# Performance work log

Measured on AMD Instinct MI355X. Metric: run time of the kernel, lower is better.

Reference implementation:

```python
import jax, jax.numpy as jnp
import numpy as np

G, N = 1024, 40            # graphs, nodes per graph (complete graphs)
SLOPE = 0.1                # leaky relu negative slope
SMAT_IDX = jnp.array([0, 1, 2, 3, 1, 4, 5, 6, 2, 5, 7, 8, 3, 6, 8, 9])


def setup_inputs() -> dict:
    key = jax.random.key(0)
    ks = jax.random.split(key, 24)

    # --- graph structure: G identical complete graphs of N nodes ---
    ii, jj = np.meshgrid(np.arange(N), np.arange(N), indexing="ij")
    mask = ii != jj
    src_l, dst_l = ii[mask], jj[mask]              # directed edges per graph
    offs = (np.arange(G) * N)[:, None]
    edge_index = np.stack([(src_l[None] + offs).ravel(),
                           (dst_l[None] + offs).ravel()]).astype(np.int64)
    iu, ju = np.triu_indices(N, 1)
    M = iu.shape[0]                                 # 780 undirected edges
    ud_edges = np.stack([iu, ju], 1).astype(np.int64)
    edge_map = np.zeros((N, N), np.int64)
    edge_map[iu, ju] = np.arange(M)
    edge_map[ju, iu] = np.arange(M)

    def w(k, shape, fan_in):
        return jax.random.normal(k, shape, jnp.float32) / np.sqrt(fan_in)

    inp = {
        "x": jax.random.normal(ks[0], (G * N, 16), jnp.float32),
        "edge_index": jnp.asarray(edge_index),
        "ud_edges": jnp.asarray(ud_edges),
        "edge_map": jnp.asarray(edge_map),
        # GCN stack 6->32->32->64
        "Wg0": w(ks[1], (6, 32), 6),   "bg0": jnp.zeros((32,), jnp.float32),
        "Wg1": w(ks[2], (32, 32), 32), "bg1": jnp.zeros((32,), jnp.float32),
        "Wg2": w(ks[3], (32, 64), 32), "bg2": jnp.zeros((64,), jnp.float32),
        # node MLP 64->64->64->10
        "Wn0": w(ks[4], (64, 64), 64), "bn0": jnp.zeros((64,), jnp.float32),
        "Wn1": w(ks[5], (64, 64), 64), "bn1": jnp.zeros((64,), jnp.float32),
        "Wn2": w(ks[6], (64, 10), 64), "bn2": jnp.zeros((10,), jnp.float32),
        # edge MLP 64->64->64->10
        "We0": w(ks[7], (64, 64), 64), "be0": jnp.zeros((64,), jnp.float32),
        "We1": w(ks[8], (64, 64), 64), "be1": jnp.zeros((64,), jnp.float32),
        "We2": w(ks[9], (64, 10), 64), "be2": jnp.zeros((10,), jnp.float32),
    }
    return inp


def _forward(x, edge_index, ud_edges, edge_map,
             Wg0, bg0, Wg1, bg1, Wg2, bg2,
             Wn0, bn0, Wn1, bn1, Wn2, bn2,
             We0, be0, We1, be1, We2, be2):
    num_nodes = x.shape[0]
    h = x[:, :6]                                   # node_feature_mode == 1
    src, dst = edge_index[0], edge_index[1]

    # GCN normalization (add_self_loops=False, edge_weight=1)
    deg = jax.ops.segment_sum(jnp.ones(src.shape[0], x.dtype), dst,
                              num_segments=num_nodes)
    dis = jnp.where(deg > 0, jax.lax.rsqrt(jnp.maximum(deg, 1e-12)), 0.0)
    norm = dis[src] * dis[dst]                     # [E]

    def gcn(h, W, b):
        m = (h @ W)[src] * norm[:, None]
        return jax.ops.segment_sum(m, dst, num_segments=num_nodes) + b

    # eval mode: dropout is identity
    h = jax.nn.leaky_relu(gcn(h, Wg0, bg0), SLOPE)
    h = jax.nn.leaky_relu(gcn(h, Wg1, bg1), SLOPE)
    h = gcn(h, Wg2, bg2)                           # [G*N, 64]

    hg = h.reshape(G, N, -1)                       # [G, N, 64]

    def mlp(z, Ws, bs):
        for W, b in zip(Ws[:-1], bs[:-1]):
            z = jax.nn.leaky_relu(z @ W + b, SLOPE)
        return z @ Ws[-1] + bs[-1]

    vp = mlp(hg, [Wn0, Wn1, Wn2], [bn0, bn1, bn2])            # [G, N, 10]
    e = hg[:, ud_edges[:, 0], :] + hg[:, ud_edges[:, 1], :]   # [G, M, 64]
    ep = mlp(e, [We0, We1, We2], [be0, be1, be2])             # [G, M, 10]

    # recover_X: diag blocks smat(vp[i]), off-diag smat(ep[edge_map[i,j]])
    epm = ep[:, edge_map, :]                                  # [G, N, N, 10]
    eye = jnp.eye(N, dtype=bool)[None, :, :, None]
    vecs = jnp.where(eye, vp[:, :, None, :], epm)             # [G, N, N, 10]
    blocks = vecs[..., SMAT_IDX].reshape(G, N, N, 4, 4)
    X = blocks.transpose(0, 1, 3, 2, 4).reshape(G, 4 * N, 4 * N)
    return h, X


def reference(x, edge_index, ud_edges, edge_map,
              Wg0, bg0, Wg1, bg1, Wg2, bg2,
              Wn0, bn0, Wn1, bn1, Wn2, bn2,
              We0, be0, We1, be1, We2, be2):
    return _forward(x, edge_index, ud_edges, edge_map,
                    Wg0, bg0, Wg1, bg1, Wg2, bg2,
                    Wn0, bn0, Wn1, bn1, Wn2, bn2,
                    We0, be0, We1, be1, We2, be2)
```

## Files before the change

### kernel.cpp

```cpp
#include <hip/hip_runtime.h>

#define G_GRAPHS 1024
#define N_NODES  40
#define M_EDGES  780
#define NUM_NODES (G_GRAPHS * N_NODES)
#define H_ELEMS  (NUM_NODES * 64)
#define X_STRIDE 160
#define X_PER_G  25600
#define SLOPE 0.1f

#define PACK_PER_MLP 9216

typedef __bf16 bf16x8 __attribute__((ext_vector_type(8)));
typedef unsigned short us8 __attribute__((ext_vector_type(8)));
typedef float f32x4 __attribute__((ext_vector_type(4)));

__device__ __forceinline__ float lrelu(float v) { return fmaxf(v, SLOPE * v); }
__device__ __forceinline__ unsigned short f2bf(float x) {
    __bf16 b = (__bf16)x;
    return __builtin_bit_cast(unsigned short, b);
}
__device__ __forceinline__ unsigned int pk2bf(float a, float b) {
    return (unsigned int)f2bf(a) | ((unsigned int)f2bf(b) << 16);
}

__global__ __launch_bounds__(256) void k_prep(const float* __restrict__ We0,
                                              const float* __restrict__ We1,
                                              const float* __restrict__ We2,
                                              const float* __restrict__ Wn0,
                                              const float* __restrict__ Wn1,
                                              const float* __restrict__ Wn2,
                                              unsigned short* __restrict__ wp) {
    int t = blockIdx.x * 256 + threadIdx.x;
    int mlp = t / PACK_PER_MLP;
    int o = t - mlp * PACK_PER_MLP;
    const float* W0 = mlp ? Wn0 : We0;
    const float* W1 = mlp ? Wn1 : We1;
    const float* W2 = mlp ? Wn2 : We2;
    float val;
    if (o < 8192) {
        const float* W = (o < 4096) ? W0 : W1;
        int idx = o & 4095;
        int j = idx & 7, l = (idx >> 3) & 63, tt = idx >> 9;
        int kt = tt & 1, mt = tt >> 1;
        int k = kt * 32 + ((l >> 4) & 3) * 8 + j;
        int m = mt * 16 + (l & 15);
        val = W[k * 64 + m];
    } else {
        int idx = o - 8192;
        int j = idx & 7, l = (idx >> 3) & 63, kt = idx >> 9;
        int k = kt * 32 + ((l >> 4) & 3) * 8 + j;
        int m = l & 15;
        val = (m < 10) ? W2[k * 10 + m] : 0.f;
    }
    wp[mlp * PACK_PER_MLP + o] = f2bf(val);
}

struct ChunkRegs {
    bf16x8 A1[4][2];
    bf16x8 A2[4][2];
    bf16x8 A3[2];
    float4 bv0[4];
    float4 bv1[4];
    float  bz[4];
};

__device__ __forceinline__ void run_pair(int R0A, int R0B, int w, int l,
                                         const float4* sh4,
                                         unsigned short* sBA,
                                         unsigned short* sBB,
                                         float* sEP,
                                         const unsigned short* sIJ,
                                         const ChunkRegs& cr) {
    const int nl = l & 15;
    const int rq = (l >> 4) & 3;
    const int rl = l >> 1;
    const int hf2 = l & 1;

    auto decode = [&](int row, int& ii, int& jj, bool& is_e, bool& is_n) {
        is_e = (row < 780);
        is_n = (row >= 800 && row < 840);
        ii = 0; jj = 0;
        if (is_e) {
            unsigned short e = sIJ[row];
            ii = e >> 8; jj = e & 255;
        } else if (is_n) {
            ii = jj = row - 800;
        }
    };
    int iiA, jjA, iiB, jjB; bool ieA, inA, ieB, inB;
    decode(R0A + rl, iiA, jjA, ieA, inA);
    decode(R0B + rl, iiB, jjB, ieB, inB);

    auto ebuild = [&](unsigned short* sB, int ii, int jj, bool is_e) {
        unsigned short tmp[32];
#pragma unroll
        for (int q = 0; q < 8; q++) {
            int u = hf2 * 8 + q;
            float4 a = sh4[ii * 16 + (u ^ ((ii & 7) << 1))];
            if (is_e) {
                float4 bq = sh4[jj * 16 + (u ^ ((jj & 7) << 1))];
                a.x += bq.x; a.y += bq.y; a.z += bq.z; a.w += bq.w;
            }
            tmp[4 * q + 0] = f2bf(a.x); tmp[4 * q + 1] = f2bf(a.y);
            tmp[4 * q + 2] = f2bf(a.z); tmp[4 * q + 3] = f2bf(a.w);
        }
        int r_sb = 32 * w + rl;
#pragma unroll
        for (int q = 0; q < 4; q++) {
            int cs = (hf2 * 4 + q) ^ (r_sb & 7);
            *(us8*)((char*)sB + r_sb * 128 + cs * 16) = *(const us8*)(tmp + 8 * q);
        }
    };
    ebuild(sBA, iiA, jjA, ieA);
    ebuild(sBB, iiB, jjB, ieB);

    auto ZB = [&](const unsigned short* s, int nt, int kt) -> bf16x8 {
        int node = 32 * w + nt * 16 + nl;
        int cs = (kt * 4 + rq) ^ (node & 7);
        return __builtin_bit_cast(bf16x8,
            *(const us8*)((const char*)s + node * 128 + cs * 16));
    };
    auto zstore = [&](unsigned short* s, int mt, int nt, const f32x4& v) {
        int node = 32 * w + nt * 16 + nl;
        int cs = (mt * 2 + (rq >> 1)) ^ (node & 7);
        uint2 u = make_uint2(pk2bf(v[0], v[1]), pk2bf(v[2], v[3]));
        *(uint2*)((char*)s + node * 128 + cs * 16 + (rq & 1) * 8) = u;
    };

    auto gemm_layer = [&](unsigned short* s, const bf16x8 A[4][2],
                          const float4* bv) {
        bf16x8 B[2][2];
#pragma unroll
        for (int nt = 0; nt < 2; nt++)
#pragma unroll
            for (int kt = 0; kt < 2; kt++) B[nt][kt] = ZB(s, nt, kt);
#pragma unroll
        for (int mt = 0; mt < 4; mt++) {
            float4 b = bv[mt];
#pragma unroll
            for (int nt = 0; nt < 2; nt++) {
                f32x4 acc = (f32x4){b.x, b.y, b.z, b.w};
                acc = __builtin_amdgcn_mfma_f32_16x16x32_bf16(A[mt][0], B[nt][0], acc, 0, 0, 0);
                acc = __builtin_amdgcn_mfma_f32_16x16x32_bf16(A[mt][1], B[nt][1], acc, 0, 0, 0);
                f32x4 z;
                z[0] = lrelu(acc[0]); z[1] = lrelu(acc[1]);
                z[2] = lrelu(acc[2]); z[3] = lrelu(acc[3]);
                zstore(s, mt, nt, z);
            }
        }
    };

    gemm_layer(sBA, cr.A1, cr.bv0);
    gemm_layer(sBB, cr.A1, cr.bv0);
    gemm_layer(sBA, cr.A2, cr.bv1);
    gemm_layer(sBB, cr.A2, cr.bv1);

    auto gemm3 = [&](unsigned short* s, int R0) {
        bf16x8 B[2][2];
#pragma unroll
        for (int nt = 0; nt < 2; nt++)
#pragma unroll
            for (int kt = 0; kt < 2; kt++) B[nt][kt] = ZB(s, nt, kt);
#pragma unroll
        for (int nt = 0; nt < 2; nt++) {
            f32x4 acc = (f32x4){cr.bz[0], cr.bz[1], cr.bz[2], cr.bz[3]};
            acc = __builtin_amdgcn_mfma_f32_16x16x32_bf16(cr.A3[0], B[nt][0], acc, 0, 0, 0);
            acc = __builtin_amdgcn_mfma_f32_16x16x32_bf16(cr.A3[1], B[nt][1], acc, 0, 0, 0);
            int rowe = R0 + nt * 16 + nl;
            bool valid = (rowe < 780) || (rowe >= 800 && rowe < 840);
            if (valid && rq < 3) {
                int epr = (rowe < 780) ? rowe : rowe - 20;
                float* p = sEP + epr * 10 + rq * 4;
                *(float2*)p = make_float2(acc[0], acc[1]);
                if (rq < 2)
                    *(float2*)(p + 2) = make_float2(acc[2], acc[3]);
            }
        }
    };
    gemm3(sBA, R0A);
    gemm3(sBB, R0B);
}

__global__ __launch_bounds__(256, 2) void k_fused(const float* __restrict__ x,
                                                  const float* __restrict__ Wg0,
                                                  const float* __restrict__ bg0,
                                                  const float* __restrict__ Wg1,
                                                  const float* __restrict__ bg1,
                                                  const float* __restrict__ Wg2,
                                                  const float* __restrict__ bg2,
                                                  const unsigned short* __restrict__ wp,
                                                  const float* __restrict__ be0,
                                                  const float* __restrict__ be1,
                                                  const float* __restrict__ be2,
                                                  const float* __restrict__ bn0,
                                                  const float* __restrict__ bn1,
                                                  const float* __restrict__ bn2,
                                                  float* __restrict__ hout,
                                                  float* __restrict__ X) {
    __shared__ __align__(16) char smem[77408];
    float* sh           = (float*)smem;
    unsigned short* sBA = (unsigned short*)(smem + 10240);
    unsigned short* sBB = (unsigned short*)(smem + 26624);
    float* sEP          = (float*)(smem + 43008);
    unsigned short* sIJ = (unsigned short*)(smem + 75808);
    float* h0  = (float*)smem;
    float* buf = (float*)(smem + 10240);
    float* h1  = (float*)(smem + 20480);
    float* h2  = (float*)(smem + 26624);
    float* P   = (float*)(smem + 43008);

    const int g = blockIdx.x;
    const int tid = threadIdx.x;
    const int l = tid & 63;
    const int w = tid >> 6;
    const float inv39 = 1.0f / 39.0f;
    const int c32 = tid & 31;
    const int c64 = tid & 63;
    const int rq = (l >> 4) & 3;

    for (int m = tid; m < 780; m += 256) {
        float tq = 6241.0f - 8.0f * (float)m;
        int i0 = (int)(0.5f * (79.0f - sqrtf(tq)));
        i0 = min(38, max(0, i0));
        int cum = 39 * i0 - ((i0 * (i0 - 1)) >> 1);
        if (cum > m) { --i0; cum = 39 * i0 - ((i0 * (i0 - 1)) >> 1); }
        else if (m - cum >= 39 - i0) { cum += 39 - i0; ++i0; }
        int jj = i0 + 1 + (m - cum);
        sIJ[m] = (unsigned short)((i0 << 8) | jj);
    }

    {
        float w0c[6], w1c[32], w2c[32];
#pragma unroll
        for (int f = 0; f < 6; f++)  w0c[f] = Wg0[f * 32 + c32];
#pragma unroll
        for (int m = 0; m < 32; m++) w1c[m] = Wg1[m * 32 + c32];
#pragma unroll
        for (int m = 0; m < 32; m++) w2c[m] = Wg2[m * 64 + c64];
        const float b0c = bg0[c32];
        const float b1c = bg1[c32];
        const float b2c = bg2[c64];

        for (int idx = tid; idx < N_NODES * 6; idx += 256) {
            int n = idx / 6, f = idx - n * 6;
            h0[idx] = x[(g * N_NODES + n) * 16 + f];
        }
        __syncthreads();

        {
            int n0 = tid >> 5;
#pragma unroll
            for (int t = 0; t < 5; t++) {
                int n = n0 + 8 * t;
                float s = 0.f;
#pragma unroll
                for (int f = 0; f < 6; f++) s += h0[n * 6 + f] * w0c[f];
                buf[n * 32 + c32] = s;
            }
        }
        __syncthreads();
        { int grp = tid >> 5; float s = 0.f;
#pragma unroll
          for (int n = grp * 5; n < grp * 5 + 5; n++) s += buf[n * 32 + c32];
          P[grp * 32 + c32] = s; }
        __syncthreads();
        { float s0 = 0.f;
#pragma unroll
          for (int grp = 0; grp < 8; grp++) s0 += P[grp * 32 + c32];
          for (int idx = tid; idx < N_NODES * 32; idx += 256)
              h1[idx] = lrelu((s0 - buf[idx]) * inv39 + b0c); }
        __syncthreads();

        {
            int n0 = tid >> 5;
#pragma unroll
            for (int t = 0; t < 5; t++) {
                int n = n0 + 8 * t;
                const float4* hp = (const float4*)(h1 + n * 32);
                float s = 0.f;
#pragma unroll
                for (int q = 0; q < 8; q++) {
                    float4 hv = hp[q];
                    s += hv.x * w1c[4 * q + 0] + hv.y * w1c[4 * q + 1]
                       + hv.z * w1c[4 * q + 2] + hv.w * w1c[4 * q + 3];
                }
                buf[n * 32 + c32] = s;
            }
        }
        __syncthreads();
        { int grp = tid >> 5; float s = 0.f;
#pragma unroll
          for (int n = grp * 5; n < grp * 5 + 5; n++) s += buf[n * 32 + c32];
          P[grp * 32 + c32] = s; }
        __syncthreads();
        { float s0 = 0.f;
#pragma unroll
          for (int grp = 0; grp < 8; grp++) s0 += P[grp * 32 + c32];
          for (int idx = tid; idx < N_NODES * 32; idx += 256)
              h2[idx] = lrelu((s0 - buf[idx]) * inv39 + b1c); }
        __syncthreads();

        {
            int n0 = tid >> 6;
#pragma unroll
            for (int t = 0; t < 10; t++) {
                int n = n0 + 4 * t;
                const float4* hp = (const float4*)(h2 + n * 32);
                float s = 0.f;
#pragma unroll
                for (int q = 0; q < 8; q++) {
                    float4 hv = hp[q];
                    s += hv.x * w2c[4 * q + 0] + hv.y * w2c[4 * q + 1]
                       + hv.z * w2c[4 * q + 2] + hv.w * w2c[4 * q + 3];
                }
                buf[n * 64 + c64] = s;
            }
        }
        __syncthreads();
        { int grp = tid >> 6; float s = 0.f;
#pragma unroll
          for (int n = grp * 10; n < grp * 10 + 10; n++) s += buf[n * 64 + c64];
          P[grp * 64 + c64] = s; }
        __syncthreads();

        { float s0 = 0.f;
#pragma unroll
          for (int grp = 0; grp < 4; grp++) s0 += P[grp * 64 + c64];
          for (int idx = tid; idx < N_NODES * 64; idx += 256) {
              float v = (s0 - buf[idx]) * inv39 + b2c;
              hout[g * N_NODES * 64 + idx] = v;
              int n = idx >> 6;
              int u = c64 >> 2;
              int us = u ^ ((n & 7) << 1);
              sh[n * 64 + us * 4 + (c64 & 3)] = v;
          } }
    }
    __syncthreads();

    const float4* sh4 = (const float4*)sh;

    auto WA = [&](const unsigned short* base, int mt, int kt) -> bf16x8 {
        return __builtin_bit_cast(bf16x8,
            *(const us8*)(base + ((mt * 2 + kt) * 64 + l) * 8));
    };
    auto loadW = [&](ChunkRegs& cr, const unsigned short* wb,
                     const float* B0, const float* B1, const float* B2) {
#pragma unroll
        for (int mt = 0; mt < 4; mt++) {
#pragma unroll
            for (int kt = 0; kt < 2; kt++) {
                cr.A1[mt][kt] = WA(wb, mt, kt);
                cr.A2[mt][kt] = WA(wb + 4096, mt, kt);
            }
            cr.bv0[mt] = *(const float4*)(B0 + mt * 16 + rq * 4);
            cr.bv1[mt] = *(const float4*)(B1 + mt * 16 + rq * 4);
        }
        cr.A3[0] = WA(wb + 8192, 0, 0);
        cr.A3[1] = WA(wb + 8192, 0, 1);
#pragma unroll
        for (int k = 0; k < 4; k++) {
            int f = rq * 4 + k;
            cr.bz[k] = (f < 10) ? B2[f] : 0.f;
        }
    };

    ChunkRegs ce;
    loadW(ce, wp, be0, be1, be2);

    for (int p = w; p < 14; p += 4) {
        int c1, c2;
        if (p < 12)       { c1 = 2 * p; c2 = 2 * p + 1; }
        else if (p == 12) { c1 = 24;    c2 = 27;        }
        else              { c1 = 25;    c2 = 26;
                            loadW(ce, wp + PACK_PER_MLP, bn0, bn1, bn2); }
        run_pair(32 * c1, 32 * c2, w, l, sh4, sBA, sBB, sEP, sIJ, ce);
    }

    __syncthreads();

    float* Xg = X + g * X_PER_G;
#pragma unroll
    for (int k = 0; k < 7; k++) {
        int b = k * 256 + tid;
        if (b < 1600) {
            int bi = b / 40;
            int bj = b - bi * 40;
            int ridx;
            if (bi == bj) {
                ridx = 780 + bi;
            } else {
                int mn = min(bi, bj), mx = max(bi, bj);
                ridx = 39 * mn - ((mn * (mn - 1)) >> 1) + (mx - mn - 1);
            }
            const float* ep = sEP + ridx * 10;
            float2 e0 = *(const float2*)(ep + 0);
            float2 e1 = *(const float2*)(ep + 2);
            float2 e2 = *(const float2*)(ep + 4);
            float2 e3 = *(const float2*)(ep + 6);
            float2 e4 = *(const float2*)(ep + 8);
            float f0 = e0.x, f1 = e0.y, f2 = e1.x, f3 = e1.y;
            float f4 = e2.x, f5 = e2.y, f6 = e3.x, f7 = e3.y;
            float f8 = e4.x, f9 = e4.y;
            float4 r0 = make_float4(f0, f1, f2, f3);
            float4 r1 = make_float4(f1, f4, f5, f6);
            float4 r2 = make_float4(f2, f5, f7, f8);
            float4 r3 = make_float4(f3, f6, f8, f9);
            float* p = Xg + (4 * bi) * X_STRIDE + 4 * bj;
            *(float4*)(p + 0 * X_STRIDE) = r0;
            *(float4*)(p + 1 * X_STRIDE) = r1;
            *(float4*)(p + 2 * X_STRIDE) = r2;
            *(float4*)(p + 3 * X_STRIDE) = r3;
        }
    }
}

extern "C" void kernel_launch(void* const* d_in, const int* in_sizes, int n_in,
                              void* d_out, int out_size, void* d_ws, size_t ws_size,
                              hipStream_t stream) {
    const float* x   = (const float*)d_in[0];
    const float* Wg0 = (const float*)d_in[4];
    const float* bg0 = (const float*)d_in[5];
    const float* Wg1 = (const float*)d_in[6];
    const float* bg1 = (const float*)d_in[7];
    const float* Wg2 = (const float*)d_in[8];
    const float* bg2 = (const float*)d_in[9];
    const float* Wn0 = (const float*)d_in[10];
    const float* bn0 = (const float*)d_in[11];
    const float* Wn1 = (const float*)d_in[12];
    const float* bn1 = (const float*)d_in[13];
    const float* Wn2 = (const float*)d_in[14];
    const float* bn2 = (const float*)d_in[15];
    const float* We0 = (const float*)d_in[16];
    const float* be0 = (const float*)d_in[17];
    const float* We1 = (const float*)d_in[18];
    const float* be1 = (const float*)d_in[19];
    const float* We2 = (const float*)d_in[20];
    const float* be2 = (const float*)d_in[21];

    float* hout = (float*)d_out;
    float* X    = hout + H_ELEMS;
    unsigned short* wp = (unsigned short*)d_ws;

    k_prep<<<72, 256, 0, stream>>>(We0, We1, We2, Wn0, Wn1, Wn2, wp);
    k_fused<<<G_GRAPHS, 256, 0, stream>>>(x, Wg0, bg0, Wg1, bg1, Wg2, bg2,
                                          wp, be0, be1, be2, bn0, bn1, bn2,
                                          hout, X);
}
```

Before: 209.0 us.

## Use 512-thread blocks with one edge chunk per wave instead of paired chunks

Doubles the block size to 8 waves. Each wave now processes a single 32-row chunk with its own LDS staging buffer, where before 4 waves each interleaved two chunks across two buffers. The GCN reductions and the X scatter loops are re-strided for 512 threads. The aim is more resident waves per CU, since LDS per block stays about the same, giving better latency hiding. The cost is a tighter per-wave register budget under the new launch bounds, which risks spills given the large weight fragments held in registers.

```diff
diff --git a/kernel.cpp b/kernel.cpp
--- a/kernel.cpp
+++ b/kernel.cpp
@@ -65,34 +65,29 @@
     float  bz[4];
 };
 
-__device__ __forceinline__ void run_pair(int R0A, int R0B, int w, int l,
-                                         const float4* sh4,
-                                         unsigned short* sBA,
-                                         unsigned short* sBB,
-                                         float* sEP,
-                                         const unsigned short* sIJ,
-                                         const ChunkRegs& cr) {
+__device__ __forceinline__ void run_chunk(int R0, int w, int l,
+                                          const float4* sh4,
+                                          unsigned short* sB,
+                                          float* sEP,
+                                          const unsigned short* sIJ,
+                                          const ChunkRegs& cr) {
     const int nl = l & 15;
     const int rq = (l >> 4) & 3;
     const int rl = l >> 1;
     const int hf2 = l & 1;
-
-    auto decode = [&](int row, int& ii, int& jj, bool& is_e, bool& is_n) {
-        is_e = (row < 780);
-        is_n = (row >= 800 && row < 840);
-        ii = 0; jj = 0;
-        if (is_e) {
-            unsigned short e = sIJ[row];
-            ii = e >> 8; jj = e & 255;
-        } else if (is_n) {
-            ii = jj = row - 800;
-        }
-    };
-    int iiA, jjA, iiB, jjB; bool ieA, inA, ieB, inB;
-    decode(R0A + rl, iiA, jjA, ieA, inA);
-    decode(R0B + rl, iiB, jjB, ieB, inB);
-
-    auto ebuild = [&](unsigned short* sB, int ii, int jj, bool is_e) {
+    const int row = R0 + rl;
+
+    const bool is_e = (row < 780);
+    const bool is_n = (row >= 800 && row < 840);
+    int ii = 0, jj = 0;
+    if (is_e) {
+        unsigned short e = sIJ[row];
+        ii = e >> 8; jj = e & 255;
+    } else if (is_n) {
+        ii = jj = row - 800;
+    }
+
+    {
         unsigned short tmp[32];
 #pragma unroll
         for (int q = 0; q < 8; q++) {
@@ -111,30 +106,27 @@
             int cs = (hf2 * 4 + q) ^ (r_sb & 7);
             *(us8*)((char*)sB + r_sb * 128 + cs * 16) = *(const us8*)(tmp + 8 * q);
         }
-    };
-    ebuild(sBA, iiA, jjA, ieA);
-    ebuild(sBB, iiB, jjB, ieB);
-
-    auto ZB = [&](const unsigned short* s, int nt, int kt) -> bf16x8 {
+    }
+
+    auto ZB = [&](int nt, int kt) -> bf16x8 {
         int node = 32 * w + nt * 16 + nl;
         int cs = (kt * 4 + rq) ^ (node & 7);
         return __builtin_bit_cast(bf16x8,
-            *(const us8*)((const char*)s + node * 128 + cs * 16));
+            *(const us8*)((const char*)sB + node * 128 + cs * 16));
     };
-    auto zstore = [&](unsigned short* s, int mt, int nt, const f32x4& v) {
+    auto zstore = [&](int mt, int nt, const f32x4& v) {
         int node = 32 * w + nt * 16 + nl;
         int cs = (mt * 2 + (rq >> 1)) ^ (node & 7);
         uint2 u = make_uint2(pk2bf(v[0], v[1]), pk2bf(v[2], v[3]));
-        *(uint2*)((char*)s + node * 128 + cs * 16 + (rq & 1) * 8) = u;
+        *(uint2*)((char*)sB + node * 128 + cs * 16 + (rq & 1) * 8) = u;
     };
 
-    auto gemm_layer = [&](unsigned short* s, const bf16x8 A[4][2],
-                          const float4* bv) {
+    auto gemm_layer = [&](const bf16x8 A[4][2], const float4* bv) {
         bf16x8 B[2][2];
 #pragma unroll
         for (int nt = 0; nt < 2; nt++)
 #pragma unroll
-            for (int kt = 0; kt < 2; kt++) B[nt][kt] = ZB(s, nt, kt);
+            for (int kt = 0; kt < 2; kt++) B[nt][kt] = ZB(nt, kt);
 #pragma unroll
         for (int mt = 0; mt < 4; mt++) {
             float4 b = bv[mt];
@@ -146,22 +138,20 @@
                 f32x4 z;
                 z[0] = lrelu(acc[0]); z[1] = lrelu(acc[1]);
                 z[2] = lrelu(acc[2]); z[3] = lrelu(acc[3]);
-                zstore(s, mt, nt, z);
+                zstore(mt, nt, z);
             }
         }
     };
 
-    gemm_layer(sBA, cr.A1, cr.bv0);
-    gemm_layer(sBB, cr.A1, cr.bv0);
-    gemm_layer(sBA, cr.A2, cr.bv1);
-    gemm_layer(sBB, cr.A2, cr.bv1);
-
-    auto gemm3 = [&](unsigned short* s, int R0) {
+    gemm_layer(cr.A1, cr.bv0);
+    gemm_layer(cr.A2, cr.bv1);
+
+    {
         bf16x8 B[2][2];
 #pragma unroll
         for (int nt = 0; nt < 2; nt++)
 #pragma unroll
-            for (int kt = 0; kt < 2; kt++) B[nt][kt] = ZB(s, nt, kt);
+            for (int kt = 0; kt < 2; kt++) B[nt][kt] = ZB(nt, kt);
 #pragma unroll
         for (int nt = 0; nt < 2; nt++) {
             f32x4 acc = (f32x4){cr.bz[0], cr.bz[1], cr.bz[2], cr.bz[3]};
@@ -177,12 +167,10 @@
                     *(float2*)(p + 2) = make_float2(acc[2], acc[3]);
             }
         }
-    };
-    gemm3(sBA, R0A);
-    gemm3(sBB, R0B);
-}
-
-__global__ __launch_bounds__(256, 2) void k_fused(const float* __restrict__ x,
+    }
+}
+
+__global__ __launch_bounds__(512, 4) void k_fused(const float* __restrict__ x,
                                                   const float* __restrict__ Wg0,
                                                   const float* __restrict__ bg0,
                                                   const float* __restrict__ Wg1,
@@ -198,16 +186,15 @@
                                                   const float* __restrict__ bn2,
                                                   float* __restrict__ hout,
                                                   float* __restrict__ X) {
-    __shared__ __align__(16) char smem[77408];
+    __shared__ __align__(16) char smem[77368];
     float* sh           = (float*)smem;
-    unsigned short* sBA = (unsigned short*)(smem + 10240);
-    unsigned short* sBB = (unsigned short*)(smem + 26624);
+    unsigned short* sB  = (unsigned short*)(smem + 10240);
     float* sEP          = (float*)(smem + 43008);
     unsigned short* sIJ = (unsigned short*)(smem + 75808);
     float* h0  = (float*)smem;
     float* buf = (float*)(smem + 10240);
     float* h1  = (float*)(smem + 20480);
-    float* h2  = (float*)(smem + 26624);
+    float* h2  = (float*)(smem + 25600);
     float* P   = (float*)(smem + 43008);
 
     const int g = blockIdx.x;
@@ -219,7 +206,7 @@
     const int c64 = tid & 63;
     const int rq = (l >> 4) & 3;
 
-    for (int m = tid; m < 780; m += 256) {
+    for (int m = tid; m < 780; m += 512) {
         float tq = 6241.0f - 8.0f * (float)m;
         int i0 = (int)(0.5f * (79.0f - sqrtf(tq)));
         i0 = min(38, max(0, i0));
@@ -242,25 +229,21 @@
         const float b1c = bg1[c32];
         const float b2c = bg2[c64];
 
-        for (int idx = tid; idx < N_NODES * 6; idx += 256) {
-            int n = idx / 6, f = idx - n * 6;
-            h0[idx] = x[(g * N_NODES + n) * 16 + f];
-        }
-        __syncthreads();
-
-        {
-            int n0 = tid >> 5;
-#pragma unroll
-            for (int t = 0; t < 5; t++) {
-                int n = n0 + 8 * t;
-                float s = 0.f;
-#pragma unroll
-                for (int f = 0; f < 6; f++) s += h0[n * 6 + f] * w0c[f];
-                buf[n * 32 + c32] = s;
-            }
-        }
-        __syncthreads();
-        { int grp = tid >> 5; float s = 0.f;
+        if (tid < 240) {
+            int n = tid / 6, f = tid - n * 6;
+            h0[tid] = x[(g * N_NODES + n) * 16 + f];
+        }
+        __syncthreads();
+
+        for (int idx = tid; idx < N_NODES * 32; idx += 512) {
+            int n = idx >> 5;
+            float s = 0.f;
+#pragma unroll
+            for (int f = 0; f < 6; f++) s += h0[n * 6 + f] * w0c[f];
+            buf[idx] = s;
+        }
+        __syncthreads();
+        if (tid < 256) { int grp = tid >> 5; float s = 0.f;
 #pragma unroll
           for (int n = grp * 5; n < grp * 5 + 5; n++) s += buf[n * 32 + c32];
           P[grp * 32 + c32] = s; }
@@ -268,28 +251,24 @@
         { float s0 = 0.f;
 #pragma unroll
           for (int grp = 0; grp < 8; grp++) s0 += P[grp * 32 + c32];
-          for (int idx = tid; idx < N_NODES * 32; idx += 256)
+          for (int idx = tid; idx < N_NODES * 32; idx += 512)
               h1[idx] = lrelu((s0 - buf[idx]) * inv39 + b0c); }
         __syncthreads();
 
-        {
-            int n0 = tid >> 5;
-#pragma unroll
-            for (int t = 0; t < 5; t++) {
-                int n = n0 + 8 * t;
-                const float4* hp = (const float4*)(h1 + n * 32);
-                float s = 0.f;
-#pragma unroll
-                for (int q = 0; q < 8; q++) {
-                    float4 hv = hp[q];
-                    s += hv.x * w1c[4 * q + 0] + hv.y * w1c[4 * q + 1]
-                       + hv.z * w1c[4 * q + 2] + hv.w * w1c[4 * q + 3];
-                }
-                buf[n * 32 + c32] = s;
-            }
-        }
-        __syncthreads();
-        { int grp = tid >> 5; float s = 0.f;
+        for (int idx = tid; idx < N_NODES * 32; idx += 512) {
+            int n = idx >> 5;
+            const float4* hp = (const float4*)(h1 + n * 32);
+            float s = 0.f;
+#pragma unroll
+            for (int q = 0; q < 8; q++) {
+                float4 hv = hp[q];
+                s += hv.x * w1c[4 * q + 0] + hv.y * w1c[4 * q + 1]
+                   + hv.z * w1c[4 * q + 2] + hv.w * w1c[4 * q + 3];
+            }
+            buf[idx] = s;
+        }
+        __syncthreads();
+        if (tid < 256) { int grp = tid >> 5; float s = 0.f;
 #pragma unroll
           for (int n = grp * 5; n < grp * 5 + 5; n++) s += buf[n * 32 + c32];
           P[grp * 32 + c32] = s; }
@@ -297,37 +276,33 @@
         { float s0 = 0.f;
 #pragma unroll
           for (int grp = 0; grp < 8; grp++) s0 += P[grp * 32 + c32];
-          for (int idx = tid; idx < N_NODES * 32; idx += 256)
+          for (int idx = tid; idx < N_NODES * 32; idx += 512)
               h2[idx] = lrelu((s0 - buf[idx]) * inv39 + b1c); }
         __syncthreads();
 
-        {
-            int n0 = tid >> 6;
-#pragma unroll
-            for (int t = 0; t < 10; t++) {
-                int n = n0 + 4 * t;
-                const float4* hp = (const float4*)(h2 + n * 32);
-                float s = 0.f;
-#pragma unroll
-                for (int q = 0; q < 8; q++) {
-                    float4 hv = hp[q];
-                    s += hv.x * w2c[4 * q + 0] + hv.y * w2c[4 * q + 1]
-                       + hv.z * w2c[4 * q + 2] + hv.w * w2c[4 * q + 3];
-                }
-                buf[n * 64 + c64] = s;
-            }
+        for (int idx = tid; idx < N_NODES * 64; idx += 512) {
+            int n = idx >> 6;
+            const float4* hp = (const float4*)(h2 + n * 32);
+            float s = 0.f;
+#pragma unroll
+            for (int q = 0; q < 8; q++) {
+                float4 hv = hp[q];
+                s += hv.x * w2c[4 * q + 0] + hv.y * w2c[4 * q + 1]
+                   + hv.z * w2c[4 * q + 2] + hv.w * w2c[4 * q + 3];
+            }
+            buf[idx] = s;
         }
         __syncthreads();
         { int grp = tid >> 6; float s = 0.f;
 #pragma unroll
-          for (int n = grp * 10; n < grp * 10 + 10; n++) s += buf[n * 64 + c64];
+          for (int n = grp * 5; n < grp * 5 + 5; n++) s += buf[n * 64 + c64];
           P[grp * 64 + c64] = s; }
         __syncthreads();
 
         { float s0 = 0.f;
 #pragma unroll
-          for (int grp = 0; grp < 4; grp++) s0 += P[grp * 64 + c64];
-          for (int idx = tid; idx < N_NODES * 64; idx += 256) {
+          for (int grp = 0; grp < 8; grp++) s0 += P[grp * 64 + c64];
+          for (int idx = tid; idx < N_NODES * 64; idx += 512) {
               float v = (s0 - buf[idx]) * inv39 + b2c;
               hout[g * N_NODES * 64 + idx] = v;
               int n = idx >> 6;
@@ -368,21 +343,18 @@
     ChunkRegs ce;
     loadW(ce, wp, be0, be1, be2);
 
-    for (int p = w; p < 14; p += 4) {
-        int c1, c2;
-        if (p < 12)       { c1 = 2 * p; c2 = 2 * p + 1; }
-        else if (p == 12) { c1 = 24;    c2 = 27;        }
-        else              { c1 = 25;    c2 = 26;
-                            loadW(ce, wp + PACK_PER_MLP, bn0, bn1, bn2); }
-        run_pair(32 * c1, 32 * c2, w, l, sh4, sBA, sBB, sEP, sIJ, ce);
+    for (int c = w; c < 28; c += 8) {
+        if (c == 25 || c == 26)
+            loadW(ce, wp + PACK_PER_MLP, bn0, bn1, bn2);
+        run_chunk(32 * c, w, l, sh4, sB, sEP, sIJ, ce);
     }
 
     __syncthreads();
 
     float* Xg = X + g * X_PER_G;
 #pragma unroll
-    for (int k = 0; k < 7; k++) {
-        int b = k * 256 + tid;
+    for (int k = 0; k < 4; k++) {
+        int b = k * 512 + tid;
         if (b < 1600) {
             int bi = b / 40;
             int bj = b - bi * 40;
@@ -443,7 +415,7 @@
     unsigned short* wp = (unsigned short*)d_ws;
 
     k_prep<<<72, 256, 0, stream>>>(We0, We1, We2, Wn0, Wn1, Wn2, wp);
-    k_fused<<<G_GRAPHS, 256, 0, stream>>>(x, Wg0, bg0, Wg1, bg1, Wg2, bg2,
+    k_fused<<<G_GRAPHS, 512, 0, stream>>>(x, Wg0, bg0, Wg1, bg1, Wg2, bg2,
                                           wp, be0, be1, be2, bn0, bn1, bn2,
                                           hout, X);
 }
```

After: 279.6 us. +33.8%, slower.

## Rebalance MLP chunk schedule across waves and keep GCN partials in registers

Applied to the files above, without the earlier changes.

The GCN layers now keep per-node products in registers and compute the partial column sums in the same pass, which removes the shared-memory scratch buffer and one barrier per layer. The edge/node MLP chunk schedule is changed from pair-based work, where waves 0 and 1 each ran four pairs, to three pairs per wave. The leftover chunks 24, 25 and 26 are then handed to waves 0, 1 and 2 through a new single-chunk path, and chunk 27 (padding rows) is skipped. This evens out per-wave load, at the cost of divergent tails and duplicated code.

```diff
diff --git a/kernel.cpp b/kernel.cpp
--- a/kernel.cpp
+++ b/kernel.cpp
@@ -182,6 +182,108 @@
     gemm3(sBB, R0B);
 }
 
+__device__ __forceinline__ void run_single(int R0, int w, int l,
+                                           const float4* sh4,
+                                           unsigned short* sBA,
+                                           float* sEP,
+                                           const unsigned short* sIJ,
+                                           const ChunkRegs& cr) {
+    const int nl = l & 15;
+    const int rq = (l >> 4) & 3;
+    const int rl = l >> 1;
+    const int hf2 = l & 1;
+    const int row = R0 + rl;
+
+    const bool is_e = (row < 780);
+    const bool is_n = (row >= 800 && row < 840);
+    int ii = 0, jj = 0;
+    if (is_e) {
+        unsigned short e = sIJ[row];
+        ii = e >> 8; jj = e & 255;
+    } else if (is_n) {
+        ii = jj = row - 800;
+    }
+
+    {
+        unsigned short tmp[32];
+#pragma unroll
+        for (int q = 0; q < 8; q++) {
+            int u = hf2 * 8 + q;
+            float4 a = sh4[ii * 16 + (u ^ ((ii & 7) << 1))];
+            if (is_e) {
+                float4 bq = sh4[jj * 16 + (u ^ ((jj & 7) << 1))];
+                a.x += bq.x; a.y += bq.y; a.z += bq.z; a.w += bq.w;
+            }
+            tmp[4 * q + 0] = f2bf(a.x); tmp[4 * q + 1] = f2bf(a.y);
+            tmp[4 * q + 2] = f2bf(a.z); tmp[4 * q + 3] = f2bf(a.w);
+        }
+        int r_sb = 32 * w + rl;
+#pragma unroll
+        for (int q = 0; q < 4; q++) {
+            int cs = (hf2 * 4 + q) ^ (r_sb & 7);
+            *(us8*)((char*)sBA + r_sb * 128 + cs * 16) = *(const us8*)(tmp + 8 * q);
+        }
+    }
+
+    auto ZB = [&](int nt, int kt) -> bf16x8 {
+        int node = 32 * w + nt * 16 + nl;
+        int cs = (kt * 4 + rq) ^ (node & 7);
+        return __builtin_bit_cast(bf16x8,
+            *(const us8*)((const char*)sBA + node * 128 + cs * 16));
+    };
+    auto zstore = [&](int mt, int nt, const f32x4& v) {
+        int node = 32 * w + nt * 16 + nl;
+        int cs = (mt * 2 + (rq >> 1)) ^ (node & 7);
+        uint2 u = make_uint2(pk2bf(v[0], v[1]), pk2bf(v[2], v[3]));
+        *(uint2*)((char*)sBA + node * 128 + cs * 16 + (rq & 1) * 8) = u;
+    };
+    auto gemm_layer = [&](const bf16x8 A[4][2], const float4* bv) {
+        bf16x8 B[2][2];
+#pragma unroll
+        for (int nt = 0; nt < 2; nt++)
+#pragma unroll
+            for (int kt = 0; kt < 2; kt++) B[nt][kt] = ZB(nt, kt);
+#pragma unroll
+        for (int mt = 0; mt < 4; mt++) {
+            float4 b = bv[mt];
+#pragma unroll
+            for (int nt = 0; nt < 2; nt++) {
+                f32x4 acc = (f32x4){b.x, b.y, b.z, b.w};
+                acc = __builtin_amdgcn_mfma_f32_16x16x32_bf16(A[mt][0], B[nt][0], acc, 0, 0, 0);
+                acc = __builtin_amdgcn_mfma_f32_16x16x32_bf16(A[mt][1], B[nt][1], acc, 0, 0, 0);
+                f32x4 z;
+                z[0] = lrelu(acc[0]); z[1] = lrelu(acc[1]);
+                z[2] = lrelu(acc[2]); z[3] = lrelu(acc[3]);
+                zstore(mt, nt, z);
+            }
+        }
+    };
+    gemm_layer(cr.A1, cr.bv0);
+    gemm_layer(cr.A2, cr.bv1);
+    {
+        bf16x8 B[2][2];
+#pragma unroll
+        for (int nt = 0; nt < 2; nt++)
+#pragma unroll
+            for (int kt = 0; kt < 2; kt++) B[nt][kt] = ZB(nt, kt);
+#pragma unroll
+        for (int nt = 0; nt < 2; nt++) {
+            f32x4 acc = (f32x4){cr.bz[0], cr.bz[1], cr.bz[2], cr.bz[3]};
+            acc = __builtin_amdgcn_mfma_f32_16x16x32_bf16(cr.A3[0], B[nt][0], acc, 0, 0, 0);
+            acc = __builtin_amdgcn_mfma_f32_16x16x32_bf16(cr.A3[1], B[nt][1], acc, 0, 0, 0);
+            int rowe = R0 + nt * 16 + nl;
+            bool valid = (rowe < 780) || (rowe >= 800 && rowe < 840);
+            if (valid && rq < 3) {
+                int epr = (rowe < 780) ? rowe : rowe - 20;
+                float* p = sEP + epr * 10 + rq * 4;
+                *(float2*)p = make_float2(acc[0], acc[1]);
+                if (rq < 2)
+                    *(float2*)(p + 2) = make_float2(acc[2], acc[3]);
+            }
+        }
+    }
+}
+
 __global__ __launch_bounds__(256, 2) void k_fused(const float* __restrict__ x,
                                                   const float* __restrict__ Wg0,
                                                   const float* __restrict__ bg0,
@@ -198,14 +300,13 @@
                                                   const float* __restrict__ bn2,
                                                   float* __restrict__ hout,
                                                   float* __restrict__ X) {
-    __shared__ __align__(16) char smem[77408];
+    __shared__ __align__(16) char smem[77368];
     float* sh           = (float*)smem;
     unsigned short* sBA = (unsigned short*)(smem + 10240);
     unsigned short* sBB = (unsigned short*)(smem + 26624);
     float* sEP          = (float*)(smem + 43008);
     unsigned short* sIJ = (unsigned short*)(smem + 75808);
     float* h0  = (float*)smem;
-    float* buf = (float*)(smem + 10240);
     float* h1  = (float*)(smem + 20480);
     float* h2  = (float*)(smem + 26624);
     float* P   = (float*)(smem + 43008);
@@ -242,38 +343,40 @@
         const float b1c = bg1[c32];
         const float b2c = bg2[c64];
 
-        for (int idx = tid; idx < N_NODES * 6; idx += 256) {
-            int n = idx / 6, f = idx - n * 6;
-            h0[idx] = x[(g * N_NODES + n) * 16 + f];
+        if (tid < 240) {
+            int n = tid / 6, f = tid - n * 6;
+            h0[tid] = x[(g * N_NODES + n) * 16 + f];
         }
         __syncthreads();
 
+        float breg[10];
+        const int n0 = tid >> 5;
+
         {
-            int n0 = tid >> 5;
+            float psum = 0.f;
 #pragma unroll
             for (int t = 0; t < 5; t++) {
                 int n = n0 + 8 * t;
                 float s = 0.f;
 #pragma unroll
                 for (int f = 0; f < 6; f++) s += h0[n * 6 + f] * w0c[f];
-                buf[n * 32 + c32] = s;
-            }
+                breg[t] = s; psum += s;
+            }
+            P[n0 * 32 + c32] = psum;
         }
         __syncthreads();
-        { int grp = tid >> 5; float s = 0.f;
-#pragma unroll
-          for (int n = grp * 5; n < grp * 5 + 5; n++) s += buf[n * 32 + c32];
-          P[grp * 32 + c32] = s; }
+        {
+            float s0 = 0.f;
+#pragma unroll
+            for (int grp = 0; grp < 8; grp++) s0 += P[grp * 32 + c32];
+#pragma unroll
+            for (int t = 0; t < 5; t++)
+                h1[(n0 + 8 * t) * 32 + c32] = lrelu((s0 - breg[t]) * inv39 + b0c);
+        }
         __syncthreads();
-        { float s0 = 0.f;
-#pragma unroll
-          for (int grp = 0; grp < 8; grp++) s0 += P[grp * 32 + c32];
-          for (int idx = tid; idx < N_NODES * 32; idx += 256)
-              h1[idx] = lrelu((s0 - buf[idx]) * inv39 + b0c); }
-        __syncthreads();
 
         {
-            int n0 = tid >> 5;
+            float psum = 0.f;
 #pragma unroll
             for (int t = 0; t < 5; t++) {
                 int n = n0 + 8 * t;
@@ -285,27 +388,27 @@
                     s += hv.x * w1c[4 * q + 0] + hv.y * w1c[4 * q + 1]
                        + hv.z * w1c[4 * q + 2] + hv.w * w1c[4 * q + 3];
                 }
-                buf[n * 32 + c32] = s;
-            }
+                breg[t] = s; psum += s;
+            }
+            P[n0 * 32 + c32] = psum;
         }
         __syncthreads();
-        { int grp = tid >> 5; float s = 0.f;
-#pragma unroll
-          for (int n = grp * 5; n < grp * 5 + 5; n++) s += buf[n * 32 + c32];
-          P[grp * 32 + c32] = s; }
+        {
+            float s0 = 0.f;
+#pragma unroll
+            for (int grp = 0; grp < 8; grp++) s0 += P[grp * 32 + c32];
+#pragma unroll
+            for (int t = 0; t < 5; t++)
+                h2[(n0 + 8 * t) * 32 + c32] = lrelu((s0 - breg[t]) * inv39 + b1c);
+        }
         __syncthreads();
-        { float s0 = 0.f;
-#pragma unroll
-          for (int grp = 0; grp < 8; grp++) s0 += P[grp * 32 + c32];
-          for (int idx = tid; idx < N_NODES * 32; idx += 256)
-              h2[idx] = lrelu((s0 - buf[idx]) * inv39 + b1c); }
-        __syncthreads();
-
+
+        const int n02 = tid >> 6;
         {
-            int n0 = tid >> 6;
+            float psum = 0.f;
 #pragma unroll
             for (int t = 0; t < 10; t++) {
-                int n = n0 + 4 * t;
+                int n = n02 + 4 * t;
                 const float4* hp = (const float4*)(h2 + n * 32);
                 float s = 0.f;
 #pragma unroll
@@ -314,27 +417,25 @@
                     s += hv.x * w2c[4 * q + 0] + hv.y * w2c[4 * q + 1]
                        + hv.z * w2c[4 * q + 2] + hv.w * w2c[4 * q + 3];
                 }
-                buf[n * 64 + c64] = s;
-            }
+                breg[t] = s; psum += s;
+            }
+            P[n02 * 64 + c64] = psum;
         }
         __syncthreads();
-        { int grp = tid >> 6; float s = 0.f;
-#pragma unroll
-          for (int n = grp * 10; n < grp * 10 + 10; n++) s += buf[n * 64 + c64];
-          P[grp * 64 + c64] = s; }
-        __syncthreads();
-
-        { float s0 = 0.f;
-#pragma unroll
-          for (int grp = 0; grp < 4; grp++) s0 += P[grp * 64 + c64];
-          for (int idx = tid; idx < N_NODES * 64; idx += 256) {
-              float v = (s0 - buf[idx]) * inv39 + b2c;
-              hout[g * N_NODES * 64 + idx] = v;
-              int n = idx >> 6;
-              int u = c64 >> 2;
-              int us = u ^ ((n & 7) << 1);
-              sh[n * 64 + us * 4 + (c64 & 3)] = v;
-          } }
+        {
+            float s0 = 0.f;
+#pragma unroll
+            for (int grp = 0; grp < 4; grp++) s0 += P[grp * 64 + c64];
+#pragma unroll
+            for (int t = 0; t < 10; t++) {
+                int n = n02 + 4 * t;
+                float v = (s0 - breg[t]) * inv39 + b2c;
+                hout[g * N_NODES * 64 + n * 64 + c64] = v;
+                int u = c64 >> 2;
+                int us = u ^ ((n & 7) << 1);
+                sh[n * 64 + us * 4 + (c64 & 3)] = v;
+            }
+        }
     }
     __syncthreads();
 
@@ -368,13 +469,19 @@
     ChunkRegs ce;
     loadW(ce, wp, be0, be1, be2);
 
-    for (int p = w; p < 14; p += 4) {
-        int c1, c2;
-        if (p < 12)       { c1 = 2 * p; c2 = 2 * p + 1; }
-        else if (p == 12) { c1 = 24;    c2 = 27;        }
-        else              { c1 = 25;    c2 = 26;
-                            loadW(ce, wp + PACK_PER_MLP, bn0, bn1, bn2); }
-        run_pair(32 * c1, 32 * c2, w, l, sh4, sBA, sBB, sEP, sIJ, ce);
+#pragma unroll
+    for (int t = 0; t < 3; t++) {
+        int c1 = 2 * w + 8 * t;
+        run_pair(32 * c1, 32 * (c1 + 1), w, l, sh4, sBA, sBB, sEP, sIJ, ce);
+    }
+    if (w == 0) {
+        run_single(32 * 24, w, l, sh4, sBA, sEP, sIJ, ce);
+    } else if (w == 1) {
+        loadW(ce, wp + PACK_PER_MLP, bn0, bn1, bn2);
+        run_single(32 * 25, w, l, sh4, sBA, sEP, sIJ, ce);
+    } else if (w == 2) {
+        loadW(ce, wp + PACK_PER_MLP, bn0, bn1, bn2);
+        run_single(32 * 26, w, l, sh4, sBA, sEP, sIJ, ce);
     }
 
     __syncthreads();
```

After: 204.3 us. -2.3%, faster.
